# Kernel optimization log

Measured on AMD Instinct MI355X. Metric: run time of the kernel, lower is better.

Reference implementation:

```python
import jax, jax.numpy as jnp
import numpy as np

# ---- problem constants (from init_kwargs / grids) ----
R, NX, NV = 64, 32768, 16384
LX, VMAX = 1.0, 8.0
DX = LX / NX
DV = 2.0 * VMAX / NV
DT = 1e-3
AE, AI = 1.0, 1836.0
ZE, ZI = -1.0, 1.0
OMEGA_C_TAU = 1.0
OMEGA_P_TAU = 1.0
NU_E, NU_I = 1.0, 0.04
XS = jnp.asarray((np.arange(NX) + 0.5) * DX - LX / 2, jnp.float32)
VS = jnp.asarray(-VMAX + (np.arange(NV) + 0.5) * DV, jnp.float32)
V_PLUS = jnp.where(VS > 0, VS, 0.0)
V_MINUS = jnp.where(VS < 0, VS, 0.0)
NU_SHAPE = jnp.ones(NX, jnp.float32)                     # collision_frequency_shape_func
_g = jnp.exp(-0.5 * (XS / (0.1 * LX)) ** 2)
GSHAPE = (_g / (jnp.sum(_g) * DX)).astype(jnp.float32)   # flux_source_shape_func


def _maxwellian(A):
    return jnp.sqrt(A / (2.0 * jnp.pi)) * jnp.exp(-A * VS ** 2 / 2.0)


def _pad(K, g):
    # AbsorbingWall: zero ghost cells
    return jnp.pad(K, ((0, 0), (g, g)))


def _dV_mats(V):
    dV = jnp.diff(V, axis=1) / DV
    z = jnp.zeros((R, 1), V.dtype)
    Vl = V @ jnp.concatenate([z, dV], axis=1).T * DV
    Vr = V @ jnp.concatenate([dV, z], axis=1).T * DV
    return Vl, Vr


def _poisson(rho):
    # 1D Gauss law: dE/dx = omega_p_tau^2 * rho_c, zero-mean gauge
    E = OMEGA_P_TAU ** 2 * jnp.cumsum(rho) * DX
    return E - jnp.mean(E)


def _flux_out_ion(Xi, Si, Vi):
    f_edge = (Xi[:, -1] @ Si) @ Vi            # (Nv,)
    return jnp.sum(V_PLUS * f_edge) * DV


def _K_rhs(K, V, E, A, Z, nu0, flux_out):
    vpm = (V_PLUS[None, :] * V) @ V.T * DV    # V @ diag(v+) @ V.T * dv, (r,r)
    vmm = (V_MINUS[None, :] * V) @ V.T * DV
    Vl, Vr = _dV_mats(V)
    Kb = _pad(K, 2)                           # (r, Nx+4)
    # upwind flux at Nx+1 interfaces
    flux = vpm @ Kb[:, 1:-2] + vmm @ Kb[:, 2:-1]
    v_flux_diff = jnp.diff(flux, axis=1) / DX
    fac = OMEGA_C_TAU * Z / A
    Ep = jnp.where(fac * E > 0, fac * E, 0.0)[None, :]
    Em = jnp.where(fac * E < 0, fac * E, 0.0)[None, :]
    E_flux = Vl @ (K * Ep) + Vr @ (K * Em)
    gamma = flux_out * GSHAPE
    n = K.T @ V.sum(1) * DV                   # (Nx,)
    nu = nu0 * NU_SHAPE
    VM = V @ _maxwellian(A) * DV              # (r,)
    coll = (n * nu + gamma)[None, :] * VM[:, None] - K * nu[None, :]
    return -v_flux_diff - E_flux + coll


def _S_rhs(S, X, V, E, A, Z, nu0, flux_out):
    vpm = (V_PLUS[None, :] * V) @ V.T * DV
    vmm = (V_MINUS[None, :] * V) @ V.T * DV
    K = _pad((X.T @ S).T, 1)                  # (r, Nx+2)
    Klm = X @ (jnp.diff(K[:, :-1], axis=1) / DX).T * DX
    Krm = X @ (jnp.diff(K[:, 1:], axis=1) / DX).T * DX
    v_term = Klm @ vpm.T + Krm @ vmm.T
    Vl, Vr = _dV_mats(V)
    fac = OMEGA_C_TAU * Z / A
    Epm = X @ (jnp.where(fac * E > 0, fac * E, 0.0)[:, None] * X.T) * DX
    Emm = X @ (jnp.where(fac * E < 0, fac * E, 0.0)[:, None] * X.T) * DX
    E_term = Epm @ S @ Vl.T + Emm @ S @ Vr.T
    gamma = flux_out * GSHAPE
    n = X.T @ (S @ V.sum(1)) * DV             # (Nx,)
    nu = nu0 * NU_SHAPE
    Xng = X @ (n * nu + gamma) * DX           # (r,)
    Xnm = X @ (nu[:, None] * X.T) * DX
    VM = V @ _maxwellian(A) * DV
    coll = Xng[:, None] * VM[None, :] - Xnm @ S
    return v_term + E_term - coll


def _L_rhs(L, X, E, A, Z, nu0, flux_out):
    Vt, St = jnp.linalg.qr(L.T)
    S = St.T * DV ** 0.5
    V = Vt.T / DV ** 0.5
    K = _pad((X.T @ S).T, 1)
    Klm = X @ (jnp.diff(K[:, :-1], axis=1) / DX).T * DX
    Krm = X @ (jnp.diff(K[:, 1:], axis=1) / DX).T * DX
    v_flux = V_PLUS[None, :] * (Klm @ V) + V_MINUS[None, :] * (Krm @ V)
    fac = OMEGA_C_TAU * Z / A
    Epm = X @ (jnp.where(fac * E > 0, fac * E, 0.0)[:, None] * X.T) * DX
    Emm = X @ (jnp.where(fac * E < 0, fac * E, 0.0)[:, None] * X.T) * DX
    Lb = _pad(L, 2)                           # (r, Nv+4)
    flux = Epm @ Lb[:, 1:-2] + Emm @ Lb[:, 2:-1]   # (r, Nv+1)
    E_flux = jnp.diff(flux, axis=1) / DV
    gamma = flux_out * GSHAPE
    n = X.T @ L.sum(1) * DV
    nu = nu0 * NU_SHAPE
    Xng = X @ (gamma + n * nu) * DX
    Xnm = X @ (nu[:, None] * X.T) * DX
    M = _maxwellian(A)
    coll = Xng[:, None] * M[None, :] - Xnm @ L
    return -v_flux - E_flux + coll


def _forward(Xe, Se, Ve, Xi, Si, Vi):
    # ---- K step (rk1 = forward Euler) ----
    flux_out = _flux_out_ion(Xi, Si, Vi)
    Ke = (Xe.T @ Se).T
    Ki = (Xi.T @ Si).T
    rho = ZE * (Ke.T @ Ve.sum(1)) * DV + ZI * (Ki.T @ Vi.sum(1)) * DV
    E = _poisson(rho)
    Ke = Ke + DT * _K_rhs(Ke, Ve, E, AE, ZE, NU_E, flux_out)
    Ki = Ki + DT * _K_rhs(Ki, Vi, E, AI, ZI, NU_I, flux_out)
    Qe, Re_ = jnp.linalg.qr(Ke.T)
    Xe, Se = Qe.T / DX ** 0.5, Re_ * DX ** 0.5
    Qi, Ri_ = jnp.linalg.qr(Ki.T)
    Xi, Si = Qi.T / DX ** 0.5, Ri_ * DX ** 0.5
    # ---- S step ----
    flux_out = _flux_out_ion(Xi, Si, Vi)
    rho = ZE * (Xe.T @ (Se @ Ve.sum(1))) * DV + ZI * (Xi.T @ (Si @ Vi.sum(1))) * DV
    E = _poisson(rho)
    Se = Se + DT * _S_rhs(Se, Xe, Ve, E, AE, ZE, NU_E, flux_out)
    Si = Si + DT * _S_rhs(Si, Xi, Vi, E, AI, ZI, NU_I, flux_out)
    # ---- L step ----
    flux_out = _flux_out_ion(Xi, Si, Vi)
    Le = Se @ Ve
    Li = Si @ Vi
    rho = ZE * (Xe.T @ Le.sum(1)) * DV + ZI * (Xi.T @ Li.sum(1)) * DV
    E = _poisson(rho)
    Le = Le + DT * _L_rhs(Le, Xe, E, AE, ZE, NU_E, flux_out)
    Li = Li + DT * _L_rhs(Li, Xi, E, AI, ZI, NU_I, flux_out)
    Qe, Re_ = jnp.linalg.qr(Le.T)
    Se, Ve = Re_.T * DV ** 0.5, Qe.T / DV ** 0.5
    Qi, Ri_ = jnp.linalg.qr(Li.T)
    Si, Vi = Ri_.T * DV ** 0.5, Qi.T / DV ** 0.5
    return jnp.stack([jnp.concatenate([Xe, Se, Ve], axis=1),
                      jnp.concatenate([Xi, Si, Vi], axis=1)])


def setup_inputs() -> dict:
    key = jax.random.key(0)
    ks = jax.random.split(key, 6)

    def ortho_x(k):
        Q, _ = jnp.linalg.qr(jax.random.normal(k, (NX, R), jnp.float32))
        return Q.T / DX ** 0.5

    def ortho_v(k):
        Q, _ = jnp.linalg.qr(jax.random.normal(k, (NV, R), jnp.float32))
        return Q.T / DV ** 0.5

    def s_mat(k):
        return 0.1 * jnp.eye(R, dtype=jnp.float32) + 0.01 * jax.random.normal(k, (R, R), jnp.float32)

    return {
        "Xe": ortho_x(ks[0]), "Se": s_mat(ks[1]), "Ve": ortho_v(ks[2]),
        "Xi": ortho_x(ks[3]), "Si": s_mat(ks[4]), "Vi": ortho_v(ks[5]),
    }


def reference(Xe, Se, Ve, Xi, Si, Vi):
    return _forward(Xe, Se, Ve, Xi, Si, Vi)
```

## Files before the change

kernel.cpp:

```cpp
#include <hip/hip_runtime.h>
#include <math.h>

#define NXC 32768
#define NVC 16384
#define OUTWC (NXC + 64 + NVC)

static constexpr float DXf   = 1.0f/32768.0f;
static constexpr float DVf   = 16.0f/16384.0f;
static constexpr float DTf   = 1e-3f;
static constexpr float VMAXf = 8.0f;
static constexpr float INV2PI= 0.15915494309189535f;

#define PS_V 16576
#define PS_X 8256
#define PS_E 8192

__global__ __launch_bounds__(1024) void k_gshape(float* __restrict__ g){
  __shared__ float red[1024];
  int t = threadIdx.x;
  float s = 0.f;
  for (int i = t; i < NXC; i += 1024){
    float x = (i + 0.5f)*DXf - 0.5f;
    float xx = x*10.0f;
    float gv = expf(-0.5f*xx*xx);
    g[i] = gv; s += gv;
  }
  red[t] = s; __syncthreads();
  for (int o = 512; o > 0; o >>= 1){ if (t < o) red[t] += red[t+o]; __syncthreads(); }
  float norm = 1.0f/(red[0]*DXf);
  for (int i = t; i < NXC; i += 1024) g[i] *= norm;
}

__global__ __launch_bounds__(256) void k_vstatsf(const float* __restrict__ V0, const float* __restrict__ V1,
                                                 float* __restrict__ part){
  __shared__ float Vt[64][67];
  int sp = blockIdx.y;
  const float* V = sp ? V1 : V0;
  float Amax = sp ? 1836.0f : 1.0f;
  int blk = blockIdx.x;
  int nbk = gridDim.x;
  int chunk = NVC/nbk;
  int c0b = blk*chunk;
  int tid = threadIdx.x;
  int ta = tid >> 4, tb = tid & 15;
  int a0 = ta*4, b0 = tb*4;
  float acc0[4][4]={{0}}, acc1[4][4]={{0}}, accp[4][4]={{0}}, accm[4][4]={{0}};
  float vsv[4]={0,0,0,0}, vvm[4]={0,0,0,0}, vwv[4]={0,0,0,0};
  float fm = sqrtf(Amax*INV2PI);
  int r0s = tid/65, c0s = tid%65;
  for (int t0 = 0; t0 < chunk; t0 += 64){
    int c0 = c0b + t0;
    {
      int r = r0s, cc = c0s;
      for (int i = tid; i < 64*65; i += 256){
        int c = c0 - 1 + cc;
        Vt[r][cc] = (c >= 0 && c < NVC) ? V[(size_t)r*NVC + c] : 0.f;
        cc += 256 - 65*3; r += 3;
        if (cc >= 65){ }
        break;
      }
      for (int i = tid; i < 64*65; i += 256){
        int rr = i/65, ccc = i%65;
        int c = c0 - 1 + ccc;
        Vt[rr][ccc] = (c >= 0 && c < NVC) ? V[(size_t)rr*NVC + c] : 0.f;
      }
    }
    __syncthreads();
    for (int jj = 0; jj < 64; ++jj){
      int j = c0 + jj;
      float vs = -VMAXf + (j + 0.5f)*DVf;
      float wpj = (vs > 0.f ? vs : 0.f)*DVf;
      float wmj = (vs < 0.f ? vs : 0.f)*DVf;
      float av[4], bv[4], bm[4];
      #pragma unroll
      for (int k=0;k<4;k++){ av[k]=Vt[a0+k][jj+1]; bv[k]=Vt[b0+k][jj+1]; bm[k]=Vt[b0+k][jj]; }
      float lag = (j >= 1) ? 1.f : 0.f;
      #pragma unroll
      for (int ka=0;ka<4;ka++){
        #pragma unroll
        for (int kb=0;kb<4;kb++){
          float p = av[ka]*bv[kb];
          acc0[ka][kb] += p;
          accp[ka][kb] += p*wpj;
          accm[ka][kb] += p*wmj;
          acc1[ka][kb] += lag*av[ka]*bm[kb];
        }
      }
      if (tb == 0){
        float mv = fm*expf(-0.5f*Amax*vs*vs)*DVf;
        #pragma unroll
        for (int k=0;k<4;k++){
          vsv[k] += av[k];
          vvm[k] += av[k]*mv;
          vwv[k] += av[k]*wpj;
        }
      }
    }
    __syncthreads();
  }
  float* pb = part + (size_t)(sp*nbk+blk)*PS_V;
  #pragma unroll
  for (int ka=0;ka<4;ka++){
    #pragma unroll
    for (int kb=0;kb<4;kb++){
      int idx = (a0+ka)*64 + (b0+kb);
      pb[idx]        = acc0[ka][kb];
      pb[4096+idx]   = acc1[ka][kb];
      pb[8192+idx]   = accp[ka][kb];
      pb[12288+idx]  = accm[ka][kb];
    }
  }
  if (tb == 0){
    #pragma unroll
    for (int k=0;k<4;k++){
      pb[16384 + a0+k] = vsv[k];
      pb[16448 + a0+k] = vvm[k];
      pb[16512 + a0+k] = vwv[k];
    }
// ... 75 lines not shown
    int c0 = c0b+t0;
    for (int i=tid;i<64*64;i+=256){
      int r=i>>6, cc=i&63;
      Xt[r][cc] = X[(size_t)r*pitch + c0+cc];
    }
    if (tid < 64) Ew[tid] = E[c0+tid]*fac;
    __syncthreads();
    for (int jj=0;jj<64;jj++){
      float w0 = Ew[jj];
      float wp = (w0>0.f?w0:0.f)*DXf, wm = (w0<0.f?w0:0.f)*DXf;
      float av[4],bv[4];
      #pragma unroll
      for (int k=0;k<4;k++){ av[k]=Xt[a0+k][jj]; bv[k]=Xt[b0+k][jj]; }
      #pragma unroll
      for (int ka=0;ka<4;ka++){
        #pragma unroll
        for (int kb=0;kb<4;kb++){
          float p = av[ka]*bv[kb];
          accp[ka][kb] += p*wp;
          accm[ka][kb] += p*wm;
        }
      }
    }
    __syncthreads();
  }
  float* pb = part + (size_t)(sp*nbk+blk)*PS_E;
  #pragma unroll
  for (int ka=0;ka<4;ka++){
    #pragma unroll
    for (int kb=0;kb<4;kb++){
      int idx = (a0+ka)*64 + (b0+kb);
      pb[idx] = accp[ka][kb];
      pb[4096+idx] = accm[ka][kb];
    }
  }
}

__global__ __launch_bounds__(256) void k_reduce32f(const float* __restrict__ part, int nb, int ps,
                                                   float* __restrict__ dst){
  int sp = blockIdx.y;
  int i = blockIdx.x*256 + threadIdx.x;
  if (i < ps){
    float s = 0.f;
    for (int b=0;b<nb;b++) s += part[(size_t)(sp*nb+b)*ps + i];
    dst[(size_t)sp*ps + i] = s;
  }
}

__global__ __launch_bounds__(256) void k_prep1(
  const float* __restrict__ Ve, const float* __restrict__ Vi,
  const float* __restrict__ Se, const float* __restrict__ Si, const float* __restrict__ Xi,
  const float* __restrict__ VDe, const float* __restrict__ VDi,
  float* __restrict__ Vle, float* __restrict__ Vre, float* __restrict__ Vli, float* __restrict__ Vri,
  float* __restrict__ VleT, float* __restrict__ VreT, float* __restrict__ VliT, float* __restrict__ VriT,
  float* __restrict__ ae, float* __restrict__ ai, float* __restrict__ fluxg)
{
  int t = threadIdx.x;
  const float* g0e = VDe; const float* g1e = VDe+4096;
  const float* g0i = VDi; const float* g1i = VDi+4096;
  const float* sVe = VDe+16384; const float* sVi = VDi+16384;
  const float* wvi = VDi+16512;
  for (int i=t;i<4096;i+=256){
    int a=i>>6, b=i&63;
    int it = b*64+a;
    float v0a=Ve[(size_t)a*NVC], v0b=Ve[(size_t)b*NVC];
    float vea=Ve[(size_t)a*NVC+NVC-1], veb=Ve[(size_t)b*NVC+NVC-1];
    float vle = (g0e[i] - v0a*v0b) - g1e[i];
    float vre = g1e[it] - g0e[i] + vea*veb;
    Vle[i] = vle; VleT[it] = vle;
    Vre[i] = vre; VreT[it] = vre;
    float w0a=Vi[(size_t)a*NVC], w0b=Vi[(size_t)b*NVC];
    float wea=Vi[(size_t)a*NVC+NVC-1], web=Vi[(size_t)b*NVC+NVC-1];
    float vli = (g0i[i] - w0a*w0b) - g1i[i];
    float vri = g1i[it] - g0i[i] + wea*web;
    Vli[i] = vli; VliT[it] = vli;
    Vri[i] = vri; VriT[it] = vri;
  }
  __shared__ float red[64];
  if (t < 64){
    float s1=0.f,s2=0.f,tr=0.f;
    for (int q=0;q<64;q++){
      s1 += Se[t*64+q]*sVe[q];
      s2 += Si[t*64+q]*sVi[q];
      tr += Xi[(size_t)q*NXC + (NXC-1)]*Si[q*64+t];
    }
    ae[t]=s1; ai[t]=s2; red[t]=tr*wvi[t];
  }
  __syncthreads();
  if (t==0){ float s=0.f; for (int r=0;r<64;r++) s+=red[r]; fluxg[0]=s; }
}

__global__ __launch_bounds__(256) void k_prep2(const float* __restrict__ Sce, const float* __restrict__ Sci,
    const float* __restrict__ VDe, const float* __restrict__ VDi, const float* __restrict__ XiN,
    const float* __restrict__ XDe, const float* __restrict__ XDi,
    float* __restrict__ ae, float* __restrict__ ai,
    float* __restrict__ Xnge, float* __restrict__ Xngi, float* __restrict__ fluxg)
{
  const float* sVe = VDe+16384; const float* sVi = VDi+16384; const float* wvi = VDi+16512;
  __shared__ float red[64];
  int t=threadIdx.x;
  if (t<64){
    float s1=0.f,s2=0.f,tr=0.f;
    for (int q=0;q<64;q++){
      s1 += Sce[t*64+q]*sVe[q];
      s2 += Sci[t*64+q]*sVi[q];
      tr += XiN[(size_t)q*OUTWC + (NXC-1)]*Sci[q*64+t];
    }
    ae[t]=s1; ai[t]=s2; red[t]=tr*wvi[t];
  }
  __syncthreads();
  if (t==0){ float s=0.f; for(int r=0;r<64;r++) s+=red[r]; fluxg[1]=s; }
  __syncthreads();
  if (t<64){
    float y1=0.f,y2=0.f;
    for (int q=0;q<64;q++){
      y1 += XDe[t*64+q]*ae[q];
      y2 += XDi[t*64+q]*ai[q];
    }
    float f = fluxg[1];
    Xnge[t] = 1.0f *DXf*DVf*y1 + f*XDe[8192+t];
    Xngi[t] = 0.04f*DXf*DVf*y2 + f*XDi[8192+t];
  }
}

__global__ __launch_bounds__(256) void k_prep3(const float* __restrict__ S2e, const float* __restrict__ S2i,
    const float* __restrict__ VDe, const float* __restrict__ VDi, const float* __restrict__ XiN,
    const float* __restrict__ XDe, const float* __restrict__ XDi,
    float* __restrict__ HTe, float* __restrict__ HTi,
    float* __restrict__ ae, float* __restrict__ ai,
    float* __restrict__ Xnge, float* __restrict__ Xngi, float* __restrict__ fluxg)
{
  const float* sVe = VDe+16384; const float* sVi = VDi+16384; const float* wvi = VDi+16512;
  const float* Ge = XDe; const float* Gi = XDi;
  const float* XGe = XDe+8192; const float* XGi = XDi+8192;
  __shared__ float red[64];
  int t=threadIdx.x;
  for (int i=t;i<4096;i+=256){
    int it = (i&63)*64 + (i>>6);
    HTe[it] = XDe[4096+i];
    HTi[it] = XDi[4096+i];
  }
  if (t<64){
    float s1=0.f,s2=0.f,tr=0.f;
    for (int q=0;q<64;q++){
      s1 += S2e[t*64+q]*sVe[q];
      s2 += S2i[t*64+q]*sVi[q];
      tr += XiN[(size_t)q*OUTWC + (NXC-1)]*S2i[q*64+t];
    }
    ae[t]=s1; ai[t]=s2; red[t]=tr*wvi[t];
  }
  __syncthreads();
  if (t==0){ float s=0.f; for(int r=0;r<64;r++) s+=red[r]; fluxg[2]=s; }
  __syncthreads();
  if (t<64){
    float y1=0.f,y2=0.f;
    for (int q=0;q<64;q++){ y1 += Ge[t*64+q]*ae[q]; y2 += Gi[t*64+q]*ai[q]; }
    float f3 = fluxg[2];
    Xnge[t] = 1.0f *DXf*DVf*y1 + f3*XGe[t];
    Xngi[t] = 0.04f*DXf*DVf*y2 + f3*XGi[t];
  }
}

__global__ __launch_bounds__(256) void k_rho(const float* __restrict__ Xe, int pe,
                                             const float* __restrict__ Xi, int pi,
                                             const float* __restrict__ ae, const float* __restrict__ ai,
                                             float* __restrict__ rho){
  int x = blockIdx.x*256 + threadIdx.x;
  float s = 0.f;
  for (int r=0;r<64;r++) s += ai[r]*Xi[(size_t)r*pi + x] - ae[r]*Xe[(size_t)r*pe + x];
  rho[x] = DVf*s;
}

__global__ __launch_bounds__(1024) void k_poisson(const float* __restrict__ rho, float* __restrict__ E){
  __shared__ float wsum[16];
  __shared__ float bsum[16];
  int t = threadIdx.x;
  int base = t*32;
  float loc[32];
  float run = 0.f;
  #pragma unroll
  for (int i=0;i<32;i++){ run += rho[base+i]; loc[i]=run; }
  float v = run;
  for (int off=1; off<64; off<<=1){
    float u = __shfl_up(v, off, 64);
    if ((t&63) >= off) v += u;
  }
  int wave = t>>6;
  if ((t&63)==63) wsum[wave] = v;
  __syncthreads();
  if (t==0){
    float a=0.f;
    for (int w0=0;w0<16;w0++){ float x=wsum[w0]; wsum[w0]=a; a+=x; }
  }
  __syncthreads();
  float offset = wsum[wave] + (v - run);
  float msum = 0.f;
  #pragma unroll
  for (int i=0;i<32;i++){ float e = DXf*(offset + loc[i]); loc[i]=e; msum += e; }
  float rs2 = msum;
  for (int off=32; off>0; off>>=1) rs2 += __shfl_down(rs2, off, 64);
  if ((t&63)==0) bsum[wave]=rs2;
  __syncthreads();
  if (t==0){ float a=0.f; for(int w0=0;w0<16;w0++) a+=bsum[w0]; bsum[0]=a; }
  __syncthreads();
  float mean = bsum[0]/(float)NXC;
  #pragma unroll
  for (int i=0;i<32;i++) E[base+i] = loc[i]-mean;
}

struct KArg { const float *X, *S, *VD, *VlT, *VrT; float nu, fac; float* Kout; };
__global__ __launch_bounds__(256) void k_kstepf(KArg k0, KArg k1,
    const float* __restrict__ E, const float* __restrict__ gsh, const float* __restrict__ fluxg)
{
  KArg A = blockIdx.y ? k1 : k0;
  __shared__ float Sl[64*65];
  __shared__ __align__(16) float Xt[64*36];
  __shared__ __align__(16) float Kt[64*36];
  __shared__ float sVs[64], VMs[64];
  int x0 = blockIdx.x*32;
  int tid = threadIdx.x;
  for (int i=tid;i<4096;i+=256) Sl[(i>>6)*65+(i&63)] = A.S[i];
  for (int i=tid;i<64*36;i+=256){
    int r=i/36, cc=i%36; int x = x0-1+cc;
    Xt[i] = (cc<34 && x>=0 && x<NXC)? A.X[(size_t)r*NXC+x] : 0.f;
  }
  if (tid<64){ sVs[tid]=A.VD[16384+tid]; VMs[tid]=A.VD[16448+tid]; }
  __syncthreads();
  for (int u=tid; u<576; u+=256){
    int q=u/9, cc0=(u%9)*4;
    float ax=0.f, ay=0.f, az=0.f, aw=0.f;
    for (int p=0;p<64;p++){
      float s = Sl[p*65+q];
      float4 xv = *reinterpret_cast<const float4*>(&Xt[p*36+cc0]);
      ax += s*xv.x; ay += s*xv.y; az += s*xv.z; aw += s*xv.w;
    }
    float4 o; o.x=ax; o.y=ay; o.z=az; o.w=aw;
    *reinterpret_cast<float4*>(&Kt[q*36+cc0]) = o;
  }
  __syncthreads();
  int r = tid & 63, w8 = (tid>>6)*8;
  float fo = fluxg[0];
  const float DTDX = DTf/DXf;
  const float* __restrict__ vpmT = A.VD + 8192;
  const float* __restrict__ vmmT = A.VD + 12288;
  const float* __restrict__ VlT  = A.VlT;
  const float* __restrict__ VrT  = A.VrT;
  float acc[8], nacc[8], epv[8], emv[8];
  #pragma unroll
  for (int c=0;c<8;c++){
    int x = x0 + w8 + c;
    float Ex = A.fac*E[x];
    epv[c] = DTf*(Ex>0.f?Ex:0.f); emv[c] = DTf*(Ex<0.f?Ex:0.f);
    acc[c]=0.f; nacc[c]=0.f;
  }
  #pragma unroll 2
  for (int q=0;q<64;q++){
    float vp_ = DTDX*vpmT[q*64+r];
    float vm_ = DTDX*vmmT[q*64+r];
    float vl  = VlT[q*64+r];
    float vr  = VrT[q*64+r];
    float sq  = sVs[q];
    float w0 = vm_ - vp_;
    const float4 kA = *reinterpret_cast<const float4*>(&Kt[q*36 + w8]);
    const float4 kB = *reinterpret_cast<const float4*>(&Kt[q*36 + w8 + 4]);
    const float2 kC = *reinterpret_cast<const float2*>(&Kt[q*36 + w8 + 8]);
    float kseg[10] = {kA.x,kA.y,kA.z,kA.w,kB.x,kB.y,kB.z,kB.w,kC.x,kC.y};
    #pragma unroll
    for (int c=0;c<8;c++){
      float kk0 = kseg[c+1];
      float t = w0 - (epv[c]*vl + emv[c]*vr);
      acc[c] += t*kk0 + vp_*kseg[c] - vm_*kseg[c+2];
      nacc[c] += sq*kk0;
    }
  }
  float vmr = VMs[r];
  #pragma unroll
  for (int c=0;c<8;c++){
    int x = x0 + w8 + c;
    float y = Kt[r*36 + w8 + c + 1]*(1.f - DTf*A.nu) + acc[c]
            + DTf*(nacc[c]*DVf*A.nu + fo*gsh[x])*vmr;
    A.Kout[(size_t)r*NXC + x] = y;
  }
}

struct LArg { const float *V, *S2, *ED, *XD, *HT, *Xng; float nu, Amax; float* Lout; };
__global__ __launch_bounds__(256) void k_lstepf(LArg l0, LArg l1)
{
  LArg A = blockIdx.y ? l1 : l0;
  __shared__ float S2l[64*65];
  __shared__ __align__(16) float Vt[64*36];
  __shared__ __align__(16) float Lt[64*36];
  __shared__ float xngs[64];
  int v0 = blockIdx.x*32;
  int tid = threadIdx.x;
  for (int i=tid;i<4096;i+=256) S2l[(i>>6)*65+(i&63)] = A.S2[i];
  for (int i=tid;i<64*36;i+=256){
    int r=i/36, cc=i%36; int vv = v0-1+cc;
    Vt[i] = (cc<34 && vv>=0 && vv<NVC)? A.V[(size_t)r*NVC+vv] : 0.f;
  }
  if (tid<64) xngs[tid]=A.Xng[tid];
  __syncthreads();
  for (int u=tid; u<576; u+=256){
    int rr=u/9, cc0=(u%9)*4;
    float ax=0.f, ay=0.f, az=0.f, aw=0.f;
    for (int q=0;q<64;q++){
      float s = S2l[rr*65+q];
      float4 xv = *reinterpret_cast<const float4*>(&Vt[q*36+cc0]);
      ax += s*xv.x; ay += s*xv.y; az += s*xv.z; aw += s*xv.w;
    }
    float4 o; o.x=ax; o.y=ay; o.z=az; o.w=aw;
    *reinterpret_cast<float4*>(&Lt[rr*36+cc0]) = o;
  }
  __syncthreads();
  int r = tid & 63, w8 = (tid>>6)*8;
  const float DTDV = DTf/DVf;
  const float* __restrict__ G  = A.XD;
  const float* __restrict__ H  = A.XD + 4096;
  const float* __restrict__ HT = A.HT;
  const float* __restrict__ Ep = A.ED;
  const float* __restrict__ Em = A.ED + 4096;
  float fm = sqrtf(A.Amax*INV2PI);
  float acc[8], vpc[8], vmc[8], mvv[8];
  #pragma unroll
  for (int c=0;c<8;c++){
    int vgl = v0 + w8 + c;
    float vs = -VMAXf + (vgl+0.5f)*DVf;
    vpc[c] = vs>0.f?vs:0.f; vmc[c] = vs<0.f?vs:0.f;
    mvv[c] = fm*expf(-0.5f*A.Amax*vs*vs);
    acc[c] = 0.f;
  }
  #pragma unroll 2
  for (int q=0;q<64;q++){
    float g  = G[q*64+r];
    float h  = HT[q*64+r];
    float ht = H[q*64+r];
    float ep = Ep[q*64+r];
    float em = Em[q*64+r];
    float gh = DTf*(g-h), hg = DTf*(ht-g);
    float dep = DTDV*ep, dem = DTDV*em;
    float b0 = -DTf*A.nu*DXf*g - (dep - dem);
    const float4 lA = *reinterpret_cast<const float4*>(&Lt[q*36 + w8]);
    const float4 lB = *reinterpret_cast<const float4*>(&Lt[q*36 + w8 + 4]);
    const float2 lC = *reinterpret_cast<const float2*>(&Lt[q*36 + w8 + 8]);
    float lseg[10] = {lA.x,lA.y,lA.z,lA.w,lB.x,lB.y,lB.z,lB.w,lC.x,lC.y};
    #pragma unroll
    for (int c=0;c<8;c++){
      float t = b0 - (vpc[c]*gh + vmc[c]*hg);
      acc[c] += t*lseg[c+1] + dep*lseg[c] - dem*lseg[c+2];
    }
  }
  float xr = xngs[r];
  #pragma unroll
  for (int c=0;c<8;c++){
    int vgl = v0 + w8 + c;
    float y = Lt[r*36 + w8 + c + 1] + acc[c] + DTf*xr*mvv[c];
    A.Lout[(size_t)r*NVC + vgl] = y;
  }
}

struct SPArg { const float *S, *XD, *ED, *Vl, *Vr, *VD; float nu; float* P; };
__global__ __launch_bounds__(256) void k_sprod(SPArg ea, SPArg ia){
  SPArg A = blockIdx.z ? ia : ea;
  int p  = blockIdx.y;
  int r0 = blockIdx.x*16;
  __shared__ float Sl[4096];
  __shared__ float Mb[16*65];
  __shared__ float M2[64*65];
  __shared__ float Tt[16*65];
  int tid = threadIdx.x;
  const float* G  = A.XD;
  const float* H  = A.XD + 4096;
  const float* Ep = A.ED;
  const float* Em = A.ED + 4096;
  for (int i=tid;i<4096;i+=256) Sl[i] = A.S[i];
  for (int i=tid;i<1024;i+=256){
    int rr=i>>6, c=i&63, r=r0+rr;
    float m;
    if      (p==0) m = G[r*64+c]-H[r*64+c];
    else if (p==1) m = H[c*64+r]-G[r*64+c];
    else if (p==2) m = Ep[r*64+c];
    else if (p==3) m = Em[r*64+c];
    else           m = G[r*64+c];
    Mb[rr*65+c]=m;
  }
  __syncthreads();
  int rr = tid>>4, b0 = (tid&15)*4;
  float acc[4]={0.f,0.f,0.f,0.f};
  for (int c=0;c<64;c++){
    float m = Mb[rr*65+c];
    #pragma unroll
    for (int k=0;k<4;k++) acc[k] += m*Sl[c*64+b0+k];
  }
  if (p==4){
    float s = A.nu*DXf;
    #pragma unroll
    for (int k=0;k<4;k++) A.P[(size_t)p*4096 + (r0+rr)*64 + b0+k] = s*acc[k];
    return;
  }
  #pragma unroll
  for (int k=0;k<4;k++) Tt[rr*65+b0+k]=acc[k];
  if (p<2){
    const float* src = (p==0)? A.VD+8192 : A.VD+12288;
    for (int i=tid;i<4096;i+=256){ int c=i>>6,b=i&63; M2[c*65+b]=src[i]; }
  } else {
    const float* src = (p==2)? A.Vl : A.Vr;
    for (int i=tid;i<4096;i+=256){ int b=i>>6,c=i&63; M2[c*65+b]=src[i]; }
  }
  __syncthreads();
// ... 184 lines not shown
  for (int i=tid;i<4096;i+=512){
    int r=i>>6, q2=i&63;
    Q.SolveM[i] = (q2<=r)? (Dv[r]*Lw[q2*65+r]*Q.invQ) : 0.f;
    if (Q.mode==0){
      Q.Sout[i] = (q2>=r)? (Dv[r]*Lg[r*65+q2]*Q.scaleS) : 0.f;
    } else {
      Q.Sout[(size_t)r*Q.outPitch + q2] = (r>=q2)? (Dv[q2]*Lg[q2*65+r]*Q.scaleS) : 0.f;
    }
  }
}

__global__ __launch_bounds__(256) void k_qformf(const float* __restrict__ A0, const float* __restrict__ A1,
    int n, const float* __restrict__ M0, const float* __restrict__ M1,
    float* __restrict__ O0, float* __restrict__ O1, int pitch)
{
  int sp = blockIdx.y >> 2;
  const float* A = sp ? A1 : A0;
  const float* M = sp ? M1 : M0;
  float* Out = sp ? O1 : O0;
  int x = blockIdx.x*256 + threadIdx.x;
  int r0 = (blockIdx.y & 3)*16;
  float acc[16];
  #pragma unroll
  for (int rr=0;rr<16;rr++) acc[rr]=0.f;
  for (int q=0;q<64;q++){
    float aq = A[(size_t)q*n + x];
    #pragma unroll
    for (int rr=0;rr<16;rr++) acc[rr] += M[(r0+rr)*64 + q]*aq;
  }
  #pragma unroll
  for (int rr=0;rr<16;rr++) Out[(size_t)(r0+rr)*pitch + x] = acc[rr];
}

extern "C" void kernel_launch(void* const* d_in, const int* in_sizes, int n_in,
                              void* d_out, int out_size, void* d_ws, size_t ws_size,
                              hipStream_t stream)
{
  (void)in_sizes; (void)n_in; (void)out_size; (void)ws_size;
  const float* Xe = (const float*)d_in[0];
  const float* Se = (const float*)d_in[1];
  const float* Ve = (const float*)d_in[2];
  const float* Xi = (const float*)d_in[3];
  const float* Si = (const float*)d_in[4];
  const float* Vi = (const float*)d_in[5];
  float* out = (float*)d_out;
  float* w = (float*)d_ws;

  size_t o = 0;
  auto alloc = [&](size_t nn){ size_t r=o; o += (nn+63)&~(size_t)63; return r; };
  size_t F_VD = alloc(2*PS_V);
  size_t F_XD = alloc(2*PS_X);
  size_t F_ED = alloc(2*PS_E);
  size_t F_VL_E = alloc(4096), F_VR_E = alloc(4096), F_VL_I = alloc(4096), F_VR_I = alloc(4096);
  size_t F_VLT_E = alloc(4096), F_VRT_E = alloc(4096), F_VLT_I = alloc(4096), F_VRT_I = alloc(4096);
  size_t F_HT_E = alloc(4096), F_HT_I = alloc(4096);
  size_t F_SC_E = alloc(4096), F_SC_I = alloc(4096), F_S2_E = alloc(4096), F_S2_I = alloc(4096);
  size_t F_SOLVE_E = alloc(4096), F_SOLVE_I = alloc(4096);
  size_t F_AE = alloc(64), F_AI = alloc(64), F_XNGE = alloc(64), F_XNGI = alloc(64);
  size_t F_FLUX = alloc(64);
  size_t F_GSH = alloc(NXC);
  size_t F_RHO = alloc(NXC);
  size_t F_E   = alloc(NXC);
  size_t F_KE = alloc((size_t)64*NXC);
  size_t F_KI = alloc((size_t)64*NXC);
  size_t F_LE = F_KE;
  size_t F_LI = F_KI;
  size_t F_PART = alloc(1060864);
  size_t F_GQR = alloc(16384);
  float* Gqr = w + F_GQR;
  float* part = w + F_PART;
  float* vpart = w + F_KE;
  float* xpart = w + F_KE;
  float* epart = w + F_KE;
  float* Pbuf  = w + F_KE;
  const float* VDe = w + F_VD;
  const float* VDi = w + F_VD + PS_V;
  const float* XDe = w + F_XD;
  const float* XDi = w + F_XD + PS_X;
  const float* EDe = w + F_ED;
  const float* EDi = w + F_ED + PS_E;

  float sqDX = sqrtf(DXf), isqDX = 1.f/sqrtf(DXf);
  float sqDV = sqrtf(DVf), isqDV = 1.f/sqrtf(DVf);
  const float NUE = 1.0f, NUI = 0.04f;
  const float FACE = -1.0f, FACI = 1.0f/1836.0f;

  k_vstatsf<<<dim3(128,2),256,0,stream>>>(Ve, Vi, vpart);
  k_reduce32f<<<dim3((PS_V+255)/256,2),256,0,stream>>>(vpart, 128, PS_V, w+F_VD);
  k_gshape<<<1,1024,0,stream>>>(w+F_GSH);
  k_prep1<<<1,256,0,stream>>>(Ve, Vi, Se, Si, Xi, VDe, VDi,
                              w+F_VL_E, w+F_VR_E, w+F_VL_I, w+F_VR_I,
                              w+F_VLT_E, w+F_VRT_E, w+F_VLT_I, w+F_VRT_I,
                              w+F_AE, w+F_AI, w+F_FLUX);
  k_rho<<<NXC/256,256,0,stream>>>(Xe, NXC, Xi, NXC, w+F_AE, w+F_AI, w+F_RHO);
  k_poisson<<<1,1024,0,stream>>>(w+F_RHO, w+F_E);
  KArg ke{Xe, Se, VDe, w+F_VLT_E, w+F_VRT_E, NUE, FACE, w+F_KE};
  KArg ki{Xi, Si, VDi, w+F_VLT_I, w+F_VRT_I, NUI, FACI, w+F_KI};
  k_kstepf<<<dim3(NXC/32,2),256,0,stream>>>(ke, ki, w+F_E, w+F_GSH, w+F_FLUX);
  k_gramf<<<dim3(128,2),256,0,stream>>>(w+F_KE, w+F_KI, NXC, part);
  k_reduce32f<<<dim3(16,2),256,0,stream>>>(part, 128, 4096, Gqr);
  {
    QArgs qe{Gqr,        w+F_KE, NXC, sqDX, isqDX, w+F_SOLVE_E, w+F_SC_E, 0, 0};
    QArgs qi{Gqr+4096,   w+F_KI, NXC, sqDX, isqDX, w+F_SOLVE_I, w+F_SC_I, 0, 0};
    k_qr<<<2,512,0,stream>>>(qe, qi);
  }
  k_qformf<<<dim3(NXC/256,8),256,0,stream>>>(w+F_KE, w+F_KI, NXC, w+F_SOLVE_E, w+F_SOLVE_I,
                                             out, out + (size_t)64*OUTWC, OUTWC);
  k_xstatsf<<<dim3(128,2),256,0,stream>>>(out, out + (size_t)64*OUTWC, OUTWC, w+F_GSH, xpart);
  k_reduce32f<<<dim3((PS_X+255)/256,2),256,0,stream>>>(xpart, 128, PS_X, w+F_XD);
  k_prep2<<<1,256,0,stream>>>(w+F_SC_E, w+F_SC_I, VDe, VDi, out + (size_t)64*OUTWC,
                              XDe, XDi,
                              w+F_AE, w+F_AI, w+F_XNGE, w+F_XNGI, w+F_FLUX);
  k_rho<<<NXC/256,256,0,stream>>>(out, OUTWC, out + (size_t)64*OUTWC, OUTWC, w+F_AE, w+F_AI, w+F_RHO);
  k_poisson<<<1,1024,0,stream>>>(w+F_RHO, w+F_E);
  k_eweightf<<<dim3(128,2),256,0,stream>>>(out, out + (size_t)64*OUTWC, OUTWC, w+F_E, FACE, FACI, epart);
  k_reduce32f<<<dim3((PS_E+255)/256,2),256,0,stream>>>(epart, 128, PS_E, w+F_ED);
  {
    SPArg spe{w+F_SC_E, XDe, EDe, w+F_VL_E, w+F_VR_E, VDe, NUE, Pbuf};
    SPArg spi{w+F_SC_I, XDi, EDi, w+F_VL_I, w+F_VR_I, VDi, NUI, Pbuf + 5*4096};
    k_sprod<<<dim3(4,5,2),256,0,stream>>>(spe, spi);
  }
  k_scomb<<<dim3(16,2),256,0,stream>>>(w+F_SC_E, w+F_SC_I, Pbuf, w+F_XNGE, w+F_XNGI,
                                       VDe, VDi, w+F_S2_E, w+F_S2_I);
  k_prep3<<<1,256,0,stream>>>(w+F_S2_E, w+F_S2_I, VDe, VDi, out + (size_t)64*OUTWC,
                              XDe, XDi, w+F_HT_E, w+F_HT_I,
                              w+F_AE, w+F_AI, w+F_XNGE, w+F_XNGI, w+F_FLUX);
  k_rho<<<NXC/256,256,0,stream>>>(out, OUTWC, out + (size_t)64*OUTWC, OUTWC, w+F_AE, w+F_AI, w+F_RHO);
  k_poisson<<<1,1024,0,stream>>>(w+F_RHO, w+F_E);
  k_eweightf<<<dim3(128,2),256,0,stream>>>(out, out + (size_t)64*OUTWC, OUTWC, w+F_E, FACE, FACI, epart);
  k_reduce32f<<<dim3((PS_E+255)/256,2),256,0,stream>>>(epart, 128, PS_E, w+F_ED);
  LArg le{Ve, w+F_S2_E, EDe, XDe, w+F_HT_E, w+F_XNGE, NUE, 1.0f,    w+F_LE};
  LArg li{Vi, w+F_S2_I, EDi, XDi, w+F_HT_I, w+F_XNGI, NUI, 1836.0f, w+F_LI};
  k_lstepf<<<dim3(NVC/32,2),256,0,stream>>>(le, li);
  k_gramf<<<dim3(128,2),256,0,stream>>>(w+F_LE, w+F_LI, NVC, part);
  k_reduce32f<<<dim3(16,2),256,0,stream>>>(part, 128, 4096, Gqr);
  {
    QArgs qe{Gqr,      w+F_LE, NVC, sqDV, isqDV, w+F_SOLVE_E, out + NXC,                        OUTWC, 1};
    QArgs qi{Gqr+4096, w+F_LI, NVC, sqDV, isqDV, w+F_SOLVE_I, out + (size_t)64*OUTWC + NXC,     OUTWC, 1};
    k_qr<<<2,512,0,stream>>>(qe, qi);
  }
  k_qformf<<<dim3(NVC/256,8),256,0,stream>>>(w+F_LE, w+F_LI, NVC, w+F_SOLVE_E, w+F_SOLVE_I,
                                             out + NXC + 64, out + (size_t)64*OUTWC + NXC + 64, OUTWC);
}
```

Baseline: 889.4 us.

## Fold S and S2 into the rank-space operators before the K and L steps

Two small pre-kernels now multiply S (and S2) into the r×r operators (upwind flux, E-flux, collision terms) once, packed interleaved per (p,r) as float4/float2. The K and L step kernels then work directly on the X/V tiles and no longer form K = S^T X or L = S2 V per tile in shared memory. This removes one 64×64×32 product per block and the per-block S staging, at the cost of two extra tiny launches and more coefficient reads from global memory. The transposed copies of Vl/Vr/H are dropped, and the odd double-load loop in vstats is simplified.

```diff
diff --git a/kernel.cpp b/kernel.cpp
--- a/kernel.cpp
+++ b/kernel.cpp
@@ -47,23 +47,12 @@
   float acc0[4][4]={{0}}, acc1[4][4]={{0}}, accp[4][4]={{0}}, accm[4][4]={{0}};
   float vsv[4]={0,0,0,0}, vvm[4]={0,0,0,0}, vwv[4]={0,0,0,0};
   float fm = sqrtf(Amax*INV2PI);
-  int r0s = tid/65, c0s = tid%65;
   for (int t0 = 0; t0 < chunk; t0 += 64){
     int c0 = c0b + t0;
-    {
-      int r = r0s, cc = c0s;
-      for (int i = tid; i < 64*65; i += 256){
-        int c = c0 - 1 + cc;
-        Vt[r][cc] = (c >= 0 && c < NVC) ? V[(size_t)r*NVC + c] : 0.f;
-        cc += 256 - 65*3; r += 3;
-        if (cc >= 65){ }
-        break;
-      }
-      for (int i = tid; i < 64*65; i += 256){
-        int rr = i/65, ccc = i%65;
-        int c = c0 - 1 + ccc;
-        Vt[rr][ccc] = (c >= 0 && c < NVC) ? V[(size_t)rr*NVC + c] : 0.f;
-      }
+    for (int i = tid; i < 64*65; i += 256){
+      int r = i/65, cc = i%65;
+      int c = c0 - 1 + cc;
+      Vt[r][cc] = (c >= 0 && c < NVC) ? V[(size_t)r*NVC + c] : 0.f;
     }
     __syncthreads();
     for (int jj = 0; jj < 64; ++jj){
@@ -245,7 +234,6 @@
   const float* __restrict__ Se, const float* __restrict__ Si, const float* __restrict__ Xi,
   const float* __restrict__ VDe, const float* __restrict__ VDi,
   float* __restrict__ Vle, float* __restrict__ Vre, float* __restrict__ Vli, float* __restrict__ Vri,
-  float* __restrict__ VleT, float* __restrict__ VreT, float* __restrict__ VliT, float* __restrict__ VriT,
   float* __restrict__ ae, float* __restrict__ ai, float* __restrict__ fluxg)
 {
   int t = threadIdx.x;
@@ -258,16 +246,12 @@
     int it = b*64+a;
     float v0a=Ve[(size_t)a*NVC], v0b=Ve[(size_t)b*NVC];
     float vea=Ve[(size_t)a*NVC+NVC-1], veb=Ve[(size_t)b*NVC+NVC-1];
-    float vle = (g0e[i] - v0a*v0b) - g1e[i];
-    float vre = g1e[it] - g0e[i] + vea*veb;
-    Vle[i] = vle; VleT[it] = vle;
-    Vre[i] = vre; VreT[it] = vre;
+    Vle[i] = (g0e[i] - v0a*v0b) - g1e[i];
+    Vre[i] = g1e[it] - g0e[i] + vea*veb;
     float w0a=Vi[(size_t)a*NVC], w0b=Vi[(size_t)b*NVC];
     float wea=Vi[(size_t)a*NVC+NVC-1], web=Vi[(size_t)b*NVC+NVC-1];
-    float vli = (g0i[i] - w0a*w0b) - g1i[i];
-    float vri = g1i[it] - g0i[i] + wea*web;
-    Vli[i] = vli; VliT[it] = vli;
-    Vri[i] = vri; VriT[it] = vri;
+    Vli[i] = (g0i[i] - w0a*w0b) - g1i[i];
+    Vri[i] = g1i[it] - g0i[i] + wea*web;
   }
   __shared__ float red[64];
   if (t < 64){
@@ -319,7 +303,6 @@
 __global__ __launch_bounds__(256) void k_prep3(const float* __restrict__ S2e, const float* __restrict__ S2i,
     const float* __restrict__ VDe, const float* __restrict__ VDi, const float* __restrict__ XiN,
     const float* __restrict__ XDe, const float* __restrict__ XDi,
-    float* __restrict__ HTe, float* __restrict__ HTi,
     float* __restrict__ ae, float* __restrict__ ai,
     float* __restrict__ Xnge, float* __restrict__ Xngi, float* __restrict__ fluxg)
 {
@@ -328,11 +311,6 @@
   const float* XGe = XDe+8192; const float* XGi = XDi+8192;
   __shared__ float red[64];
   int t=threadIdx.x;
-  for (int i=t;i<4096;i+=256){
-    int it = (i&63)*64 + (i>>6);
-    HTe[it] = XDe[4096+i];
-    HTi[it] = XDi[4096+i];
-  }
   if (t<64){
     float s1=0.f,s2=0.f,tr=0.f;
     for (int q=0;q<64;q++){
@@ -401,43 +379,131 @@
   for (int i=0;i<32;i++) E[base+i] = loc[i]-mean;
 }
 
-struct KArg { const float *X, *S, *VD, *VlT, *VrT; float nu, fac; float* Kout; };
+struct FKArg { const float *S, *VD, *Vl, *Vr; float nu; float *PA, *PB; };
+__global__ __launch_bounds__(256) void k_foldK(FKArg a0, FKArg a1){
+  FKArg A = blockIdx.y ? a1 : a0;
+  __shared__ float Sl[64*65];
+  __shared__ float Mrow[4][16*65];
+  __shared__ float wv[64];
+  int tid = threadIdx.x;
+  int r0 = blockIdx.x*16;
+  const float* vpm = A.VD + 8192;
+  const float* vmm = A.VD + 12288;
+  const float* sVs = A.VD + 16384;
+  for (int i=tid;i<4096;i+=256) Sl[(i>>6)*65+(i&63)] = A.S[i];
+  for (int i=tid;i<1024;i+=256){
+    int rr=i>>6, q=i&63; int r=r0+rr;
+    Mrow[0][rr*65+q] = vpm[r*64+q];
+    Mrow[1][rr*65+q] = vmm[r*64+q];
+    Mrow[2][rr*65+q] = A.Vl[r*64+q];
+    Mrow[3][rr*65+q] = A.Vr[r*64+q];
+  }
+  __syncthreads();
+  if (tid < 64){
+    float s=0.f;
+    for (int q=0;q<64;q++) s += sVs[q]*Sl[tid*65+q];
+    wv[tid]=s;
+  }
+  __syncthreads();
+  int rr = tid>>4, pp = (tid&15)*4;
+  int r = r0+rr;
+  const float DTDX = DTf/DXf;
+  float c0[4]={0,0,0,0}, cl[4]={0,0,0,0}, cr[4]={0,0,0,0}, cp[4]={0,0,0,0}, cm[4]={0,0,0,0};
+  for (int q=0;q<64;q++){
+    float vp_ = DTDX*Mrow[0][rr*65+q];
+    float vm_ = DTDX*Mrow[1][rr*65+q];
+    float vlv = Mrow[2][rr*65+q];
+    float vrv = Mrow[3][rr*65+q];
+    float w0 = vm_ - vp_;
+    #pragma unroll
+    for (int k=0;k<4;k++){
+      float sv = Sl[(pp+k)*65+q];
+      c0[k] += w0*sv;
+      cl[k] += vlv*sv;
+      cr[k] += vrv*sv;
+      cp[k] += vp_*sv;
+      cm[k] += vm_*sv;
+    }
+  }
+  float dn = 1.f - DTf*A.nu;
+  #pragma unroll
+  for (int k=0;k<4;k++){
+    int p = pp+k;
+    float c0f = c0[k] + dn*Sl[p*65+r];
+    int qi = (p<<6) + r;
+    float4 pa; pa.x=c0f; pa.y=cp[k]; pa.z=cm[k]; pa.w=wv[p];
+    *reinterpret_cast<float4*>(&A.PA[4*qi]) = pa;
+    float2 pb; pb.x=cl[k]; pb.y=cr[k];
+    *reinterpret_cast<float2*>(&A.PB[2*qi]) = pb;
+  }
+}
+
+struct FLArg { const float *S2, *XD, *ED; float nu; float *QA, *QB; };
+__global__ __launch_bounds__(256) void k_foldL(FLArg a0, FLArg a1){
+  FLArg A = blockIdx.y ? a1 : a0;
+  __shared__ float Sl[64*65];
+  __shared__ float Hl[64*65];
+  int tid = threadIdx.x;
+  int r0 = blockIdx.x*16;
+  for (int i=tid;i<4096;i+=256){
+    Sl[(i>>6)*65+(i&63)] = A.S2[i];
+    Hl[(i>>6)*65+(i&63)] = A.XD[4096+i];
+  }
+  __syncthreads();
+  int rr = tid>>4, pp = (tid&15)*4;
+  int r = r0+rr;
+  const float DTDV = DTf/DVf;
+  float d0[4]={0,0,0,0}, dgh[4]={0,0,0,0}, dhg[4]={0,0,0,0}, dp[4]={0,0,0,0}, dm[4]={0,0,0,0};
+  for (int q=0;q<64;q++){
+    float g  = A.XD[r*64+q];
+    float ep = A.ED[r*64+q];
+    float em = A.ED[4096 + r*64+q];
+    float h  = Hl[r*65+q];
+    float ht = Hl[q*65+r];
+    float gh = DTf*(g-h), hg = DTf*(ht-g);
+    float dep = DTDV*ep, dem = DTDV*em;
+    float b0 = -DTf*A.nu*DXf*g - dep + dem;
+    #pragma unroll
+    for (int k=0;k<4;k++){
+      float sv = Sl[q*65+pp+k];
+      d0[k]  += b0*sv;
+      dgh[k] += gh*sv;
+      dhg[k] += hg*sv;
+      dp[k]  += dep*sv;
+      dm[k]  += dem*sv;
+    }
+  }
+  #pragma unroll
+  for (int k=0;k<4;k++){
+    int p = pp+k;
+    float d0f = d0[k] + Sl[r*65+p];
+    int qi = (p<<6) + r;
+    float4 qa; qa.x=d0f; qa.y=dp[k]; qa.z=dm[k]; qa.w=0.f;
+    *reinterpret_cast<float4*>(&A.QA[4*qi]) = qa;
+    float2 qb; qb.x=dgh[k]; qb.y=dhg[k];
+    *reinterpret_cast<float2*>(&A.QB[2*qi]) = qb;
+  }
+}
+
+struct KArg { const float *X, *PA, *PB, *VD; float nu, fac; float* Kout; };
 __global__ __launch_bounds__(256) void k_kstepf(KArg k0, KArg k1,
     const float* __restrict__ E, const float* __restrict__ gsh, const float* __restrict__ fluxg)
 {
   KArg A = blockIdx.y ? k1 : k0;
-  __shared__ float Sl[64*65];
   __shared__ __align__(16) float Xt[64*36];
-  __shared__ __align__(16) float Kt[64*36];
-  __shared__ float sVs[64], VMs[64];
+  __shared__ float VMs[64];
   int x0 = blockIdx.x*32;
   int tid = threadIdx.x;
-  for (int i=tid;i<4096;i+=256) Sl[(i>>6)*65+(i&63)] = A.S[i];
   for (int i=tid;i<64*36;i+=256){
     int r=i/36, cc=i%36; int x = x0-1+cc;
     Xt[i] = (cc<34 && x>=0 && x<NXC)? A.X[(size_t)r*NXC+x] : 0.f;
   }
-  if (tid<64){ sVs[tid]=A.VD[16384+tid]; VMs[tid]=A.VD[16448+tid]; }
-  __syncthreads();
-  for (int u=tid; u<576; u+=256){
-    int q=u/9, cc0=(u%9)*4;
-    float ax=0.f, ay=0.f, az=0.f, aw=0.f;
-    for (int p=0;p<64;p++){
-      float s = Sl[p*65+q];
-      float4 xv = *reinterpret_cast<const float4*>(&Xt[p*36+cc0]);
-      ax += s*xv.x; ay += s*xv.y; az += s*xv.z; aw += s*xv.w;
-    }
-    float4 o; o.x=ax; o.y=ay; o.z=az; o.w=aw;
-    *reinterpret_cast<float4*>(&Kt[q*36+cc0]) = o;
-  }
+  if (tid<64) VMs[tid]=A.VD[16448+tid];
   __syncthreads();
   int r = tid & 63, w8 = (tid>>6)*8;
   float fo = fluxg[0];
-  const float DTDX = DTf/DXf;
-  const float* __restrict__ vpmT = A.VD + 8192;
-  const float* __restrict__ vmmT = A.VD + 12288;
-  const float* __restrict__ VlT  = A.VlT;
-  const float* __restrict__ VrT  = A.VrT;
+  const float* __restrict__ PA = A.PA;
+  const float* __restrict__ PB = A.PB;
   float acc[8], nacc[8], epv[8], emv[8];
   #pragma unroll
   for (int c=0;c<8;c++){
@@ -447,71 +513,48 @@
     acc[c]=0.f; nacc[c]=0.f;
   }
   #pragma unroll 2
-  for (int q=0;q<64;q++){
-    float vp_ = DTDX*vpmT[q*64+r];
-    float vm_ = DTDX*vmmT[q*64+r];
-    float vl  = VlT[q*64+r];
-    float vr  = VrT[q*64+r];
-    float sq  = sVs[q];
-    float w0 = vm_ - vp_;
-    const float4 kA = *reinterpret_cast<const float4*>(&Kt[q*36 + w8]);
-    const float4 kB = *reinterpret_cast<const float4*>(&Kt[q*36 + w8 + 4]);
-    const float2 kC = *reinterpret_cast<const float2*>(&Kt[q*36 + w8 + 8]);
+  for (int p=0;p<64;p++){
+    int qi = (p<<6) + r;
+    float4 pa = *reinterpret_cast<const float4*>(&PA[4*qi]);
+    float2 pb = *reinterpret_cast<const float2*>(&PB[2*qi]);
+    const float4 kA = *reinterpret_cast<const float4*>(&Xt[p*36 + w8]);
+    const float4 kB = *reinterpret_cast<const float4*>(&Xt[p*36 + w8 + 4]);
+    const float2 kC = *reinterpret_cast<const float2*>(&Xt[p*36 + w8 + 8]);
     float kseg[10] = {kA.x,kA.y,kA.z,kA.w,kB.x,kB.y,kB.z,kB.w,kC.x,kC.y};
     #pragma unroll
     for (int c=0;c<8;c++){
-      float kk0 = kseg[c+1];
-      float t = w0 - (epv[c]*vl + emv[c]*vr);
-      acc[c] += t*kk0 + vp_*kseg[c] - vm_*kseg[c+2];
-      nacc[c] += sq*kk0;
+      float xv = kseg[c+1];
+      float t = pa.x - (epv[c]*pb.x + emv[c]*pb.y);
+      acc[c] += t*xv + pa.y*kseg[c] - pa.z*kseg[c+2];
+      nacc[c] += pa.w*xv;
     }
   }
   float vmr = VMs[r];
   #pragma unroll
   for (int c=0;c<8;c++){
     int x = x0 + w8 + c;
-    float y = Kt[r*36 + w8 + c + 1]*(1.f - DTf*A.nu) + acc[c]
-            + DTf*(nacc[c]*DVf*A.nu + fo*gsh[x])*vmr;
+    float y = acc[c] + DTf*(nacc[c]*DVf*A.nu + fo*gsh[x])*vmr;
     A.Kout[(size_t)r*NXC + x] = y;
   }
 }
 
-struct LArg { const float *V, *S2, *ED, *XD, *HT, *Xng; float nu, Amax; float* Lout; };
+struct LArg { const float *V, *QA, *QB, *Xng; float Amax; float* Lout; };
 __global__ __launch_bounds__(256) void k_lstepf(LArg l0, LArg l1)
 {
   LArg A = blockIdx.y ? l1 : l0;
-  __shared__ float S2l[64*65];
   __shared__ __align__(16) float Vt[64*36];
-  __shared__ __align__(16) float Lt[64*36];
   __shared__ float xngs[64];
   int v0 = blockIdx.x*32;
   int tid = threadIdx.x;
-  for (int i=tid;i<4096;i+=256) S2l[(i>>6)*65+(i&63)] = A.S2[i];
   for (int i=tid;i<64*36;i+=256){
     int r=i/36, cc=i%36; int vv = v0-1+cc;
     Vt[i] = (cc<34 && vv>=0 && vv<NVC)? A.V[(size_t)r*NVC+vv] : 0.f;
   }
   if (tid<64) xngs[tid]=A.Xng[tid];
   __syncthreads();
-  for (int u=tid; u<576; u+=256){
-    int rr=u/9, cc0=(u%9)*4;
-    float ax=0.f, ay=0.f, az=0.f, aw=0.f;
-    for (int q=0;q<64;q++){
-      float s = S2l[rr*65+q];
-      float4 xv = *reinterpret_cast<const float4*>(&Vt[q*36+cc0]);
-      ax += s*xv.x; ay += s*xv.y; az += s*xv.z; aw += s*xv.w;
-    }
-    float4 o; o.x=ax; o.y=ay; o.z=az; o.w=aw;
-    *reinterpret_cast<float4*>(&Lt[rr*36+cc0]) = o;
-  }
-  __syncthreads();
   int r = tid & 63, w8 = (tid>>6)*8;
-  const float DTDV = DTf/DVf;
-  const float* __restrict__ G  = A.XD;
-  const float* __restrict__ H  = A.XD + 4096;
-  const float* __restrict__ HT = A.HT;
-  const float* __restrict__ Ep = A.ED;
-  const float* __restrict__ Em = A.ED + 4096;
+  const float* __restrict__ QA = A.QA;
+  const float* __restrict__ QB = A.QB;
   float fm = sqrtf(A.Amax*INV2PI);
   float acc[8], vpc[8], vmc[8], mvv[8];
   #pragma unroll
@@ -523,30 +566,25 @@
     acc[c] = 0.f;
   }
   #pragma unroll 2
-  for (int q=0;q<64;q++){
-    float g  = G[q*64+r];
-    float h  = HT[q*64+r];
-    float ht = H[q*64+r];
-    float ep = Ep[q*64+r];
-    float em = Em[q*64+r];
-    float gh = DTf*(g-h), hg = DTf*(ht-g);
-    float dep = DTDV*ep, dem = DTDV*em;
-    float b0 = -DTf*A.nu*DXf*g - (dep - dem);
-    const float4 lA = *reinterpret_cast<const float4*>(&Lt[q*36 + w8]);
-    const float4 lB = *reinterpret_cast<const float4*>(&Lt[q*36 + w8 + 4]);
-    const float2 lC = *reinterpret_cast<const float2*>(&Lt[q*36 + w8 + 8]);
+  for (int p=0;p<64;p++){
+    int qi = (p<<6) + r;
+    float4 qa = *reinterpret_cast<const float4*>(&QA[4*qi]);
+    float2 qb = *reinterpret_cast<const float2*>(&QB[2*qi]);
+    const float4 lA = *reinterpret_cast<const float4*>(&Vt[p*36 + w8]);
+    const float4 lB = *reinterpret_cast<const float4*>(&Vt[p*36 + w8 + 4]);
+    const float2 lC = *reinterpret_cast<const float2*>(&Vt[p*36 + w8 + 8]);
     float lseg[10] = {lA.x,lA.y,lA.z,lA.w,lB.x,lB.y,lB.z,lB.w,lC.x,lC.y};
     #pragma unroll
     for (int c=0;c<8;c++){
-      float t = b0 - (vpc[c]*gh + vmc[c]*hg);
-      acc[c] += t*lseg[c+1] + dep*lseg[c] - dem*lseg[c+2];
+      float t = qa.x - (vpc[c]*qb.x + vmc[c]*qb.y);
+      acc[c] += t*lseg[c+1] + qa.y*lseg[c] - qa.z*lseg[c+2];
     }
   }
   float xr = xngs[r];
   #pragma unroll
   for (int c=0;c<8;c++){
     int vgl = v0 + w8 + c;
-    float y = Lt[r*36 + w8 + c + 1] + acc[c] + DTf*xr*mvv[c];
+    float y = acc[c] + DTf*xr*mvv[c];
     A.Lout[(size_t)r*NVC + vgl] = y;
   }
 }
@@ -837,8 +875,10 @@
   size_t F_XD = alloc(2*PS_X);
   size_t F_ED = alloc(2*PS_E);
   size_t F_VL_E = alloc(4096), F_VR_E = alloc(4096), F_VL_I = alloc(4096), F_VR_I = alloc(4096);
-  size_t F_VLT_E = alloc(4096), F_VRT_E = alloc(4096), F_VLT_I = alloc(4096), F_VRT_I = alloc(4096);
-  size_t F_HT_E = alloc(4096), F_HT_I = alloc(4096);
+  size_t F_PA_E = alloc(16384), F_PA_I = alloc(16384);
+  size_t F_PB_E = alloc(8192),  F_PB_I = alloc(8192);
+  size_t F_QA_E = alloc(16384), F_QA_I = alloc(16384);
+  size_t F_QB_E = alloc(8192),  F_QB_I = alloc(8192);
   size_t F_SC_E = alloc(4096), F_SC_I = alloc(4096), F_S2_E = alloc(4096), F_S2_I = alloc(4096);
   size_t F_SOLVE_E = alloc(4096), F_SOLVE_I = alloc(4096);
   size_t F_AE = alloc(64), F_AI = alloc(64), F_XNGE = alloc(64), F_XNGI = alloc(64);
@@ -875,12 +915,16 @@
   k_gshape<<<1,1024,0,stream>>>(w+F_GSH);
   k_prep1<<<1,256,0,stream>>>(Ve, Vi, Se, Si, Xi, VDe, VDi,
                               w+F_VL_E, w+F_VR_E, w+F_VL_I, w+F_VR_I,
-                              w+F_VLT_E, w+F_VRT_E, w+F_VLT_I, w+F_VRT_I,
                               w+F_AE, w+F_AI, w+F_FLUX);
+  {
+    FKArg fe{Se, VDe, w+F_VL_E, w+F_VR_E, NUE, w+F_PA_E, w+F_PB_E};
+    FKArg fi{Si, VDi, w+F_VL_I, w+F_VR_I, NUI, w+F_PA_I, w+F_PB_I};
+    k_foldK<<<dim3(4,2),256,0,stream>>>(fe, fi);
+  }
   k_rho<<<NXC/256,256,0,stream>>>(Xe, NXC, Xi, NXC, w+F_AE, w+F_AI, w+F_RHO);
   k_poisson<<<1,1024,0,stream>>>(w+F_RHO, w+F_E);
-  KArg ke{Xe, Se, VDe, w+F_VLT_E, w+F_VRT_E, NUE, FACE, w+F_KE};
-  KArg ki{Xi, Si, VDi, w+F_VLT_I, w+F_VRT_I, NUI, FACI, w+F_KI};
+  KArg ke{Xe, w+F_PA_E, w+F_PB_E, VDe, NUE, FACE, w+F_KE};
+  KArg ki{Xi, w+F_PA_I, w+F_PB_I, VDi, NUI, FACI, w+F_KI};
   k_kstepf<<<dim3(NXC/32,2),256,0,stream>>>(ke, ki, w+F_E, w+F_GSH, w+F_FLUX);
   k_gramf<<<dim3(128,2),256,0,stream>>>(w+F_KE, w+F_KI, NXC, part);
   k_reduce32f<<<dim3(16,2),256,0,stream>>>(part, 128, 4096, Gqr);
@@ -908,14 +952,19 @@
   k_scomb<<<dim3(16,2),256,0,stream>>>(w+F_SC_E, w+F_SC_I, Pbuf, w+F_XNGE, w+F_XNGI,
                                        VDe, VDi, w+F_S2_E, w+F_S2_I);
   k_prep3<<<1,256,0,stream>>>(w+F_S2_E, w+F_S2_I, VDe, VDi, out + (size_t)64*OUTWC,
-                              XDe, XDi, w+F_HT_E, w+F_HT_I,
+                              XDe, XDi,
                               w+F_AE, w+F_AI, w+F_XNGE, w+F_XNGI, w+F_FLUX);
   k_rho<<<NXC/256,256,0,stream>>>(out, OUTWC, out + (size_t)64*OUTWC, OUTWC, w+F_AE, w+F_AI, w+F_RHO);
   k_poisson<<<1,1024,0,stream>>>(w+F_RHO, w+F_E);
   k_eweightf<<<dim3(128,2),256,0,stream>>>(out, out + (size_t)64*OUTWC, OUTWC, w+F_E, FACE, FACI, epart);
   k_reduce32f<<<dim3((PS_E+255)/256,2),256,0,stream>>>(epart, 128, PS_E, w+F_ED);
-  LArg le{Ve, w+F_S2_E, EDe, XDe, w+F_HT_E, w+F_XNGE, NUE, 1.0f,    w+F_LE};
-  LArg li{Vi, w+F_S2_I, EDi, XDi, w+F_HT_I, w+F_XNGI, NUI, 1836.0f, w+F_LI};
+  {
+    FLArg fe{w+F_S2_E, XDe, EDe, NUE, w+F_QA_E, w+F_QB_E};
+    FLArg fi{w+F_S2_I, XDi, EDi, NUI, w+F_QA_I, w+F_QB_I};
+    k_foldL<<<dim3(4,2),256,0,stream>>>(fe, fi);
+  }
+  LArg le{Ve, w+F_QA_E, w+F_QB_E, w+F_XNGE, 1.0f,    w+F_LE};
+  LArg li{Vi, w+F_QA_I, w+F_QB_I, w+F_XNGI, 1836.0f, w+F_LI};
   k_lstepf<<<dim3(NVC/32,2),256,0,stream>>>(le, li);
   k_gramf<<<dim3(128,2),256,0,stream>>>(w+F_LE, w+F_LI, NVC, part);
   k_reduce32f<<<dim3(16,2),256,0,stream>>>(part, 128, 4096, Gqr);
```

After: 876.7 us. No clear change (-1.4%).
